# Optimization experiments

Hardware: AMD Instinct MI355X
Metric: run time of the kernel (lower is better)

The kernel has to match this reference:

```python
import jax, jax.numpy as jnp
import numpy as np

ALPHA = 0.2  # module hardcodes a = 0.2


def _triplet_total(outputs, labels):
    # Faithful vectorization of the nested-loop mining:
    #  - sort samples by label (stable, like python sorted with key=label)
    #  - anchor p1 = first element of each contiguous label group
    #  - positives p2 = remaining members of the group; ap = ||p1-p2||^2
    #  - negatives = every sample with a different label
    #  - per (p2, neg): add (ap - an + alpha) for an in {||p1-n||^2, ||p2-n||^2}
    #    iff ap < an and ap - an + alpha > 0  (i.e. 0 < an - ap < alpha)
    order = jnp.argsort(labels)          # stable sort, matches python sorted
    x = outputs[order]                   # [n, d]
    lab = labels[order]                  # [n]
    n = x.shape[0]
    idx = jnp.arange(n)
    is_start = jnp.concatenate([jnp.ones((1,), bool), lab[1:] != lab[:-1]])
    # index of the group-start (anchor) for every position
    anchor_of = jax.lax.cummax(jnp.where(is_start, idx, 0))

    # pairwise squared distances Dm[i,j] = ||x_i - x_j||^2
    sq = jnp.sum(x * x, axis=-1)                       # [n]
    Dm = sq[:, None] + sq[None, :] - 2.0 * (x @ x.T)   # [n, n]

    ap = Dm[anchor_of, idx]   # [n]   ||p1 - p2||^2 for each potential positive
    an1 = Dm[anchor_of, :]    # [n,n] ||p1 - neg||^2
    an2 = Dm                  # [n,n] ||p2 - neg||^2

    pos_mask = ~is_start                         # p2 ranges over non-anchor rows
    neg_mask = lab[:, None] != lab[None, :]      # negatives: different label
    valid = pos_mask[:, None] & neg_mask         # [n, n]

    def hinge(an):
        d = ap[:, None] - an
        return jnp.where((d < 0) & (d + ALPHA > 0), d + ALPHA, 0.0)

    contrib = jnp.where(valid, hinge(an1) + hinge(an2), 0.0)
    return jnp.sum(contrib)


def setup_inputs() -> dict:
    key = jax.random.key(0)
    k1, k2 = jax.random.split(key)
    N, D, C = 8192, 128, 512
    outputs = jax.random.normal(k1, (N, D), dtype=jnp.float32)
    labels = jax.random.randint(k2, (N,), 0, C, dtype=jnp.int32)
    return {"outputs": outputs, "labels": labels}


def reference(outputs, labels):
    return _triplet_total(outputs, labels)
```

## Files before the change

kernel.cpp:

```cpp
#include <hip/hip_runtime.h>
#include <limits.h>
#include <stdint.h>

#define ALPHA 0.2f
#define HALFA 0.1f
static constexpr int N = 8192;
static constexpr int D = 128;
static constexpr int C = 512;
static constexpr int BT = 128;
static constexpr int GR = D / 8;
static constexpr int SL = BT + 1;
static constexpr int MAXG = 48;
static constexpr int NB = N / BT;
static constexpr int NT1T = 512;
static constexpr int NSP = NB / 2;
static constexpr int SPB = 16;
static constexpr int GRID = 512;

#define DMASK 3.0e38f
#define EPAD  1.0e37f

using half8    = __attribute__((ext_vector_type(8))) _Float16;
using floatx16 = __attribute__((ext_vector_type(16))) float;

__device__ __forceinline__ floatx16 zerov() { floatx16 v = {0.f}; return v; }

__device__ __forceinline__ half8 cvt8(float4 v0, float4 v1) {
    half8 h;
    h[0] = (_Float16)v0.x; h[1] = (_Float16)v0.y; h[2] = (_Float16)v0.z; h[3] = (_Float16)v0.w;
    h[4] = (_Float16)v1.x; h[5] = (_Float16)v1.y; h[6] = (_Float16)v1.z; h[7] = (_Float16)v1.w;
    return h;
}

__device__ __forceinline__ float ss8(float4 v0, float4 v1) {
    return v0.x*v0.x + v0.y*v0.y + v0.z*v0.z + v0.w*v0.w
         + v1.x*v1.x + v1.y*v1.y + v1.z*v1.z + v1.w*v1.w;
}

__device__ __forceinline__ void dec_sp(int k, int t, int lenA, int& br, int& bc) {
    if (t < lenA) { br = k;      bc = k + t; }
    else          { br = 63 - k; bc = 63 - k + (t - lenA); }
}


__launch_bounds__(256)
__global__ void k_prep(const float* __restrict__ x, const int* __restrict__ labels,
                       _Float16* __restrict__ xh, float* __restrict__ sq,
                       int* __restrict__ anchorg, float* __restrict__ ap,
                       int* __restrict__ ecnt, float* __restrict__ egrid,
                       float* __restrict__ out) {
    __shared__ int sAnc[C];
    const int tid = threadIdx.x;
    if (blockIdx.x == 0 && tid == 0) out[0] = 0.f;
    for (int i = tid; i < C; i += 256) sAnc[i] = INT_MAX;
    __syncthreads();
    const int4* lab4 = (const int4*)labels;
    for (int t = tid; t < N / 4; t += 256) {
        int4 lv = lab4[t];
        int base = 4 * t;
        atomicMin(&sAnc[lv.x], base);
        atomicMin(&sAnc[lv.y], base + 1);
        atomicMin(&sAnc[lv.z], base + 2);
        atomicMin(&sAnc[lv.w], base + 3);
    }
    __syncthreads();
    if (tid < 2) {
        int c = blockIdx.x * 2 + tid;
        int a = sAnc[c];
        anchorg[c] = (a == INT_MAX) ? -1 : a;
    }

    const int r = blockIdx.x * 32 + (tid >> 3);
    const int sub = tid & 7;
    const float4* src = (const float4*)(x + (size_t)r * D) + sub * 4;
    half8* dst = (half8*)(xh + (size_t)r * D) + sub * 2;
    half8 hj[2];
    float ssj = 0.f;
#pragma unroll
    for (int i = 0; i < 2; ++i) {
        float4 v0 = src[2 * i], v1 = src[2 * i + 1];
        hj[i] = cvt8(v0, v1);
        dst[i] = hj[i];
        ssj += ss8(v0, v1);
    }
    ssj += __shfl_xor(ssj, 1); ssj += __shfl_xor(ssj, 2); ssj += __shfl_xor(ssj, 4);

    const int lab = labels[r];
    const int a = sAnc[lab];
    const float4* asrc = (const float4*)(x + (size_t)a * D) + sub * 4;
    float ssa = 0.f, dot = 0.f;
#pragma unroll
    for (int i = 0; i < 2; ++i) {
        float4 a0 = asrc[2 * i], a1 = asrc[2 * i + 1];
        half8 ha = cvt8(a0, a1);
        ssa += ss8(a0, a1);
#pragma unroll
        for (int e = 0; e < 8; ++e) dot = fmaf((float)ha[e], (float)hj[i][e], dot);
    }
    ssa += __shfl_xor(ssa, 1); ssa += __shfl_xor(ssa, 2); ssa += __shfl_xor(ssa, 4);
    dot += __shfl_xor(dot, 1); dot += __shfl_xor(dot, 2); dot += __shfl_xor(dot, 4);
    if (sub == 0) {
        float apv = ssa + ssj - 2.f * dot;
        sq[r] = ssj;
        ap[r] = apv;
        if (r != a) {
            int slot = atomicAdd(&ecnt[lab], 1);
            if (slot < MAXG) egrid[(size_t)lab * MAXG + slot] = apv + HALFA;
        }
    }
}


__launch_bounds__(512, 2)
__global__ void k_main(const _Float16* __restrict__ xh, const int* __restrict__ labels,
                       const int* __restrict__ anchor, const float* __restrict__ sq,
                       const float* __restrict__ ap, const int* __restrict__ ecnt,
                       const float* __restrict__ egrid, float* __restrict__ out) {
    __shared__ __align__(16) _Float16 BsH[GR * SL * 8];
    __shared__ __align__(16) float sge[64 * MAXG];
    __shared__ float4 rowE[BT];
    __shared__ float4 colE[2][BT];
    __shared__ int   sArow[64];
    __shared__ float sSqA[64];
    __shared__ int   sCnt[64];
    __shared__ float wsum[8];
    half8* Bs = (half8*)BsH;

    const int tid = threadIdx.x;
    const int lane = tid & 63, w = tid >> 6;
    const int m = lane & 31, q = lane >> 5;
    const int sg = tid & 15, sr0 = tid >> 4;
    float local = 0.f;
    int cnt = 0;

    const int b = blockIdx.x;
    const int c0 = (b >> 6) * 64, j1 = (b & 63) * BT;
    const int kk_sp = b >> 4, p = b & 15;
    const int lenA = 64 - kk_sp;

    half8 af[8], breg[4];
    floatx16 acc = zerov();

    if (tid < 64) {
        int c = c0 + tid;
        int a = anchor[c];
        int ar = (a < 0) ? 0 : a;
        sArow[tid] = ar;
        sSqA[tid] = sq[ar];
        int n = ecnt[c];
        sCnt[tid] = (n > MAXG) ? MAXG : n;
    }
    {
        const float4* srcv = (const float4*)(egrid + (size_t)c0 * MAXG);
        float4* dstv = (float4*)sge;
#pragma unroll
        for (int rep = 0; rep < 2; ++rep) {
            int idx = tid + rep * 512;
            if (idx < 64 * (MAXG / 4)) {
                int cls = idx / (MAXG / 4);
                int sb = (idx % (MAXG / 4)) * 4;
                int n = ecnt[c0 + cls]; n = (n > MAXG) ? MAXG : n;
                float4 v = srcv[idx];
                v.x = (sb + 0 < n) ? v.x : EPAD;
                v.y = (sb + 1 < n) ? v.y : EPAD;
                v.z = (sb + 2 < n) ? v.z : EPAD;
                v.w = (sb + 3 < n) ? v.w : EPAD;
                dstv[idx] = v;
            }
        }
    }
#pragma unroll
    for (int i = 0; i < 4; ++i)
        breg[i] = *((const half8*)(xh + (size_t)(j1 + sr0 + 32 * i) * D) + sg);
    if (tid < BT) {
        int j = j1 + tid;
        colE[0][tid] = make_float4(sq[j], __int_as_float(labels[j]), 0.f, 0.f);
    }
    __syncthreads();

    {
        int arow = sArow[(w >> 2) * 32 + m];
        const half8* aptr = (const half8*)(xh + (size_t)arow * D) + q;
#pragma unroll
        for (int k = 0; k < 8; ++k) af[k] = aptr[2 * k];
    }
#pragma unroll
    for (int i = 0; i < 4; ++i)
        Bs[sg * SL + sr0 + 32 * i] = breg[i];
    __syncthreads();

#pragma unroll
    for (int k = 0; k < 8; ++k) {
        half8 b0 = Bs[(2 * k + q) * SL + (w & 3) * 32 + m];
        acc = __builtin_amdgcn_mfma_f32_32x32x16_f16(af[k], b0, acc, 0, 0, 0);
    }

    int br0, bc0;
    dec_sp(kk_sp, p, lenA, br0, bc0);
    {
        const half8* aptr = (const half8*)(xh + (size_t)(br0 * BT + (w >> 1) * 32 + m) * D) + q;
#pragma unroll
        for (int k = 0; k < 8; ++k) af[k] = aptr[2 * k];
#pragma unroll
        for (int i = 0; i < 4; ++i)
            breg[i] = *((const half8*)(xh + (size_t)(bc0 * BT + sr0 + 32 * i) * D) + sg);
        if (tid < BT) {
            int i = br0 * BT + tid;
            int li = labels[i]; int a = anchor[li];
            float sqi = sq[i];
            float e2 = (i == a) ? -1e30f : ap[i] + HALFA - sqi;
            rowE[tid] = make_float4(e2, __int_as_float(li), sqi, 0.f);
        } else if (tid < 2 * BT) {
            int j = bc0 * BT + tid - BT;
            int lj = labels[j]; int a = anchor[lj];
            float sqj = sq[j];
            float e2 = (j == a) ? -1e30f : ap[j] + HALFA - sqj;
            colE[1][tid - BT] = make_float4(e2, __int_as_float(lj), sqj, 0.f);
        }
    }

    __builtin_amdgcn_s_setprio(1);
    {
        float4 cj = colE[0][(w & 3) * 32 + m];
        float sqj = cj.x; int labj = __float_as_int(cj.y);
#pragma unroll
        for (int rr = 0; rr < 16; ++rr) {
            int row = (w >> 2) * 32 + (rr & 3) + 8 * (rr >> 2) + 4 * q;
            float Dv = fmaf(-2.f, acc[rr], sSqA[row] + sqj);
            Dv = (labj != c0 + row) ? Dv : DMASK;
            int nf = (sCnt[row] + 3) & ~3;
            cnt += nf;
            for (int gb = 0; gb < nf; gb += 4) {
                float4 ev = *(const float4*)&sge[row * MAXG + gb];
                float u;
                u = ev.x - Dv; local += (__builtin_fabsf(u) < HALFA) ? u : -HALFA;
                u = ev.y - Dv; local += (__builtin_fabsf(u) < HALFA) ? u : -HALFA;
                u = ev.z - Dv; local += (__builtin_fabsf(u) < HALFA) ? u : -HALFA;
                u = ev.w - Dv; local += (__builtin_fabsf(u) < HALFA) ? u : -HALFA;
            }
        }
    }
    __builtin_amdgcn_s_setprio(0);
    __syncthreads();

    {
        const int wr = w >> 1, wc = w & 1;
        int cbuf = 1, cur_br = br0;

        for (int t = p; t < 65; t += SPB) {
            int br, bc; dec_sp(kk_sp, t, lenA, br, bc);
            const int i0 = br * BT;
            const bool diag = (br == bc);

            if (br != cur_br) {
                cur_br = br;
                const half8* aptr = (const half8*)(xh + (size_t)(i0 + wr * 32 + m) * D) + q;
#pragma unroll
                for (int k8 = 0; k8 < 8; ++k8) af[k8] = aptr[2 * k8];
                if (tid < BT) {
                    int i = i0 + tid;
                    int li = labels[i]; int a = anchor[li];
                    float sqi = sq[i];
                    float e2 = (i == a) ? -1e30f : ap[i] + HALFA - sqi;
                    rowE[tid] = make_float4(e2, __int_as_float(li), sqi, 0.f);
                }
            }

#pragma unroll
            for (int i = 0; i < 4; ++i)
                Bs[sg * SL + sr0 + 32 * i] = breg[i];
            __syncthreads();

            if (t + SPB < 65) {
                int brn, bcn; dec_sp(kk_sp, t + SPB, lenA, brn, bcn);
                int j0n = bcn * BT;
#pragma unroll
                for (int i = 0; i < 4; ++i)
                    breg[i] = *((const half8*)(xh + (size_t)(j0n + sr0 + 32 * i) * D) + sg);
                if (tid < BT) {
                    int j = j0n + tid;
                    int lj = labels[j]; int a = anchor[lj];
                    float sqj = sq[j];
                    float e2 = (j == a) ? -1e30f : ap[j] + HALFA - sqj;
                    colE[cbuf ^ 1][tid] = make_float4(e2, __int_as_float(lj), sqj, 0.f);
                }
            }

            __builtin_amdgcn_s_setprio(1);
            floatx16 acc0 = zerov(), acc1 = zerov();
#pragma unroll
            for (int k8 = 0; k8 < 8; ++k8) {
                half8 b0 = Bs[(2 * k8 + q) * SL + wc * 64 + m];
                half8 b1 = Bs[(2 * k8 + q) * SL + wc * 64 + 32 + m];
                acc0 = __builtin_amdgcn_mfma_f32_32x32x16_f16(af[k8], b0, acc0, 0, 0, 0);
                acc1 = __builtin_amdgcn_mfma_f32_32x32x16_f16(af[k8], b1, acc1, 0, 0, 0);
            }

            float sqjv[2], e2j[2]; int labj[2];
            { float4 cj = colE[cbuf][wc * 64 + m];      e2j[0] = cj.x; labj[0] = __float_as_int(cj.y); sqjv[0] = cj.z; }
            { float4 cj = colE[cbuf][wc * 64 + 32 + m]; e2j[1] = cj.x; labj[1] = __float_as_int(cj.y); sqjv[1] = cj.z; }

#pragma unroll
            for (int rr = 0; rr < 16; ++rr) {
                int row = wr * 32 + (rr & 3) + 8 * (rr >> 2) + 4 * q;
                float4 re = rowE[row];
                float e2i = re.x, sqi = re.z;
                int labi = __float_as_int(re.y);
#pragma unroll
                for (int tn = 0; tn < 2; ++tn) {
                    float dot = (tn == 0) ? acc0[rr] : acc1[rr];
                    bool ne = (labi != labj[tn]);
                    float u2 = fmaf(2.f, dot, e2i - sqjv[tn]);
                    local += (ne & (__builtin_fabsf(u2) < HALFA)) ? u2 : -HALFA;
                    if (!diag) {
                        float u2b = fmaf(2.f, dot, e2j[tn] - sqi);
                        local += (ne & (__builtin_fabsf(u2b) < HALFA)) ? u2b : -HALFA;
                    }
                }
            }
            __builtin_amdgcn_s_setprio(0);
            cnt += diag ? 32 : 64;
            cbuf ^= 1;
            __syncthreads();
        }
    }

    local += HALFA * (float)cnt;
#pragma unroll
    for (int off = 32; off; off >>= 1) local += __shfl_down(local, off);
    if (lane == 0) wsum[w] = local;
    __syncthreads();
    if (tid == 0) {
        float s = 0.f;
#pragma unroll
        for (int i = 0; i < 8; ++i) s += wsum[i];
        atomicAdd(out, s);
    }
}


extern "C" void kernel_launch(void* const* d_in, const int* in_sizes, int n_in,
                              void* d_out, int out_size, void* d_ws, size_t ws_size,
                              hipStream_t stream) {
    const float* x = (const float*)d_in[0];
    const int* labels = (const int*)d_in[1];
    float* out = (float*)d_out;

    char* p = (char*)d_ws;
    int* anchor = (int*)p;        p += C * 4;
    float* sq = (float*)p;        p += N * 4;
    float* ap = (float*)p;        p += N * 4;
    int* ecnt = (int*)p;          p += C * 4;
    float* egrid = (float*)p;     p += (size_t)C * MAXG * 4;
    p = (char*)(((uintptr_t)p + 255) & ~(uintptr_t)255);
    _Float16* xh = (_Float16*)p;

    hipMemsetAsync(ecnt, 0, C * 4, stream);
    k_prep<<<N / 32, 256, 0, stream>>>(x, labels, xh, sq, anchor, ap, ecnt, egrid, out);
    k_main<<<GRID, 512, 0, stream>>>(xh, labels, anchor, sq, ap, ecnt, egrid, out);
}
```

Baseline: 105.1 us.

## Fuse prep and main kernels into one persistent kernel with grid barriers

Merges the preprocessing kernel into the main kernel, using two software grid-wide barriers built on atomic counters with sleep-spin waits. The aim is to remove one kernel launch and the gap between kernels. The change also moves the ecnt zeroing into the kernel and adds memsets for the anchors and barrier counters. It depends on all 512 blocks being co-resident (512 threads, 2 blocks per CU) to avoid deadlock, and the spin barriers add their own latency. Anchors are now found with a global atomicMin instead of per-block shared atomics, and the anchor dot product now uses the fp16 copy.

New measurement: 183.3 us. 74.4% more time.

```diff
diff --git a/kernel.cpp b/kernel.cpp
--- a/kernel.cpp
+++ b/kernel.cpp
@@ -12,7 +12,6 @@
 static constexpr int SL = BT + 1;
 static constexpr int MAXG = 48;
 static constexpr int NB = N / BT;
-static constexpr int NT1T = 512;
 static constexpr int NSP = NB / 2;
 static constexpr int SPB = 16;
 static constexpr int GRID = 512;
@@ -24,98 +23,31 @@
 using floatx16 = __attribute__((ext_vector_type(16))) float;
 
 __device__ __forceinline__ floatx16 zerov() { floatx16 v = {0.f}; return v; }
-
-__device__ __forceinline__ half8 cvt8(float4 v0, float4 v1) {
-    half8 h;
-    h[0] = (_Float16)v0.x; h[1] = (_Float16)v0.y; h[2] = (_Float16)v0.z; h[3] = (_Float16)v0.w;
-    h[4] = (_Float16)v1.x; h[5] = (_Float16)v1.y; h[6] = (_Float16)v1.z; h[7] = (_Float16)v1.w;
-    return h;
-}
-
-__device__ __forceinline__ float ss8(float4 v0, float4 v1) {
-    return v0.x*v0.x + v0.y*v0.y + v0.z*v0.z + v0.w*v0.w
-         + v1.x*v1.x + v1.y*v1.y + v1.z*v1.z + v1.w*v1.w;
-}
 
 __device__ __forceinline__ void dec_sp(int k, int t, int lenA, int& br, int& bc) {
     if (t < lenA) { br = k;      bc = k + t; }
     else          { br = 63 - k; bc = 63 - k + (t - lenA); }
 }
 
-
-__launch_bounds__(256)
-__global__ void k_prep(const float* __restrict__ x, const int* __restrict__ labels,
-                       _Float16* __restrict__ xh, float* __restrict__ sq,
-                       int* __restrict__ anchorg, float* __restrict__ ap,
-                       int* __restrict__ ecnt, float* __restrict__ egrid,
-                       float* __restrict__ out) {
-    __shared__ int sAnc[C];
-    const int tid = threadIdx.x;
-    if (blockIdx.x == 0 && tid == 0) out[0] = 0.f;
-    for (int i = tid; i < C; i += 256) sAnc[i] = INT_MAX;
-    __syncthreads();
-    const int4* lab4 = (const int4*)labels;
-    for (int t = tid; t < N / 4; t += 256) {
-        int4 lv = lab4[t];
-        int base = 4 * t;
-        atomicMin(&sAnc[lv.x], base);
-        atomicMin(&sAnc[lv.y], base + 1);
-        atomicMin(&sAnc[lv.z], base + 2);
-        atomicMin(&sAnc[lv.w], base + 3);
-    }
-    __syncthreads();
-    if (tid < 2) {
-        int c = blockIdx.x * 2 + tid;
-        int a = sAnc[c];
-        anchorg[c] = (a == INT_MAX) ? -1 : a;
-    }
-
-    const int r = blockIdx.x * 32 + (tid >> 3);
-    const int sub = tid & 7;
-    const float4* src = (const float4*)(x + (size_t)r * D) + sub * 4;
-    half8* dst = (half8*)(xh + (size_t)r * D) + sub * 2;
-    half8 hj[2];
-    float ssj = 0.f;
-#pragma unroll
-    for (int i = 0; i < 2; ++i) {
-        float4 v0 = src[2 * i], v1 = src[2 * i + 1];
-        hj[i] = cvt8(v0, v1);
-        dst[i] = hj[i];
-        ssj += ss8(v0, v1);
-    }
-    ssj += __shfl_xor(ssj, 1); ssj += __shfl_xor(ssj, 2); ssj += __shfl_xor(ssj, 4);
-
-    const int lab = labels[r];
-    const int a = sAnc[lab];
-    const float4* asrc = (const float4*)(x + (size_t)a * D) + sub * 4;
-    float ssa = 0.f, dot = 0.f;
-#pragma unroll
-    for (int i = 0; i < 2; ++i) {
-        float4 a0 = asrc[2 * i], a1 = asrc[2 * i + 1];
-        half8 ha = cvt8(a0, a1);
-        ssa += ss8(a0, a1);
-#pragma unroll
-        for (int e = 0; e < 8; ++e) dot = fmaf((float)ha[e], (float)hj[i][e], dot);
-    }
-    ssa += __shfl_xor(ssa, 1); ssa += __shfl_xor(ssa, 2); ssa += __shfl_xor(ssa, 4);
-    dot += __shfl_xor(dot, 1); dot += __shfl_xor(dot, 2); dot += __shfl_xor(dot, 4);
-    if (sub == 0) {
-        float apv = ssa + ssj - 2.f * dot;
-        sq[r] = ssj;
-        ap[r] = apv;
-        if (r != a) {
-            int slot = atomicAdd(&ecnt[lab], 1);
-            if (slot < MAXG) egrid[(size_t)lab * MAXG + slot] = apv + HALFA;
-        }
-    }
+__device__ __forceinline__ void grid_barrier(int* bar) {
+    __syncthreads();
+    if (threadIdx.x == 0) {
+        __threadfence();
+        __hip_atomic_fetch_add(bar, 1, __ATOMIC_ACQ_REL, __HIP_MEMORY_SCOPE_AGENT);
+        while (__hip_atomic_load(bar, __ATOMIC_ACQUIRE, __HIP_MEMORY_SCOPE_AGENT) < GRID)
+            __builtin_amdgcn_s_sleep(8);
+        __threadfence();
+    }
+    __syncthreads();
 }
 
 
 __launch_bounds__(512, 2)
-__global__ void k_main(const _Float16* __restrict__ xh, const int* __restrict__ labels,
-                       const int* __restrict__ anchor, const float* __restrict__ sq,
-                       const float* __restrict__ ap, const int* __restrict__ ecnt,
-                       const float* __restrict__ egrid, float* __restrict__ out) {
+__global__ void k_all(const float* __restrict__ x, const int* __restrict__ labels,
+                      _Float16* __restrict__ xh, float* __restrict__ sq,
+                      unsigned* __restrict__ anchor_u, float* __restrict__ ap,
+                      int* __restrict__ ecnt, float* __restrict__ egrid,
+                      int* __restrict__ bars, float* __restrict__ out) {
     __shared__ __align__(16) _Float16 BsH[GR * SL * 8];
     __shared__ __align__(16) float sge[64 * MAXG];
     __shared__ float4 rowE[BT];
@@ -134,6 +66,51 @@
     int cnt = 0;
 
     const int b = blockIdx.x;
+
+    {
+        if (tid == 0) { ecnt[b] = 0; if (b == 0) out[0] = 0.f; }
+        const int rl = tid >> 5, l32 = tid & 31;
+        const int r = b * 16 + rl;
+        float4 v = *((const float4*)(x + (size_t)r * D) + l32);
+        union { _Float16 h[4]; uint2 u; } cv;
+        cv.h[0] = (_Float16)v.x; cv.h[1] = (_Float16)v.y;
+        cv.h[2] = (_Float16)v.z; cv.h[3] = (_Float16)v.w;
+        *((uint2*)(xh + (size_t)r * D) + l32) = cv.u;
+        float ss = v.x*v.x + v.y*v.y + v.z*v.z + v.w*v.w;
+        ss += __shfl_xor(ss, 1); ss += __shfl_xor(ss, 2); ss += __shfl_xor(ss, 4);
+        ss += __shfl_xor(ss, 8); ss += __shfl_xor(ss, 16);
+        if (l32 == 0) {
+            sq[r] = ss;
+            atomicMin(&anchor_u[labels[r]], (unsigned)r);
+        }
+    }
+    grid_barrier(&bars[0]);
+
+    {
+        const int rl = tid >> 5, l32 = tid & 31;
+        const int r = b * 16 + rl;
+        const int lab = labels[r];
+        const int a = (int)anchor_u[lab];
+        union { uint2 u; _Float16 h[4]; } ca, cr;
+        ca.u = *((const uint2*)(xh + (size_t)a * D) + l32);
+        cr.u = *((const uint2*)(xh + (size_t)r * D) + l32);
+        float dot = 0.f;
+#pragma unroll
+        for (int e = 0; e < 4; ++e) dot = fmaf((float)ca.h[e], (float)cr.h[e], dot);
+        dot += __shfl_xor(dot, 1); dot += __shfl_xor(dot, 2); dot += __shfl_xor(dot, 4);
+        dot += __shfl_xor(dot, 8); dot += __shfl_xor(dot, 16);
+        if (l32 == 0) {
+            float apv = sq[a] + sq[r] - 2.f * dot;
+            ap[r] = apv;
+            if (r != a) {
+                int slot = atomicAdd(&ecnt[lab], 1);
+                if (slot < MAXG) egrid[(size_t)lab * MAXG + slot] = apv + HALFA;
+            }
+        }
+    }
+    grid_barrier(&bars[1]);
+
+    const int* anchor = (const int*)anchor_u;
     const int c0 = (b >> 6) * 64, j1 = (b & 63) * BT;
     const int kk_sp = b >> 4, p = b & 15;
     const int lenA = 64 - kk_sp;
@@ -347,15 +324,17 @@
     float* out = (float*)d_out;
 
     char* p = (char*)d_ws;
-    int* anchor = (int*)p;        p += C * 4;
-    float* sq = (float*)p;        p += N * 4;
-    float* ap = (float*)p;        p += N * 4;
-    int* ecnt = (int*)p;          p += C * 4;
-    float* egrid = (float*)p;     p += (size_t)C * MAXG * 4;
+    unsigned* anchor_u = (unsigned*)p; p += C * 4;
+    float* sq = (float*)p;             p += N * 4;
+    float* ap = (float*)p;             p += N * 4;
+    int* ecnt = (int*)p;               p += C * 4;
+    float* egrid = (float*)p;          p += (size_t)C * MAXG * 4;
+    int* bars = (int*)p;               p += 2 * 4;
     p = (char*)(((uintptr_t)p + 255) & ~(uintptr_t)255);
     _Float16* xh = (_Float16*)p;
 
-    hipMemsetAsync(ecnt, 0, C * 4, stream);
-    k_prep<<<N / 32, 256, 0, stream>>>(x, labels, xh, sq, anchor, ap, ecnt, egrid, out);
-    k_main<<<GRID, 512, 0, stream>>>(xh, labels, anchor, sq, ap, ecnt, egrid, out);
+    hipMemsetAsync(anchor_u, 0xFF, C * 4, stream);
+    hipMemsetAsync(bars, 0, 2 * 4, stream);
+    k_all<<<GRID, 512, 0, stream>>>(x, labels, xh, sq, anchor_u, ap, ecnt, egrid,
+                                    bars, out);
 }
```
